# Kernel tuning notes

Hardware: AMD Instinct MI355X
Metric: run time of the kernel (lower is better)

Reference implementation:

```python
import jax, jax.numpy as jnp
import numpy as np

B, S, C, HEADS, EXP = 8, 1024, 256, 8, 4
H = W = 32  # S = H*W
HID = EXP * C
RATES = (1, 6, 12, 18)
EPS = 1e-5


def _conv(x, w, b=None, dilation=1, padding=0):
    out = jax.lax.conv_general_dilated(
        x, w, (1, 1), [(padding, padding), (padding, padding)],
        rhs_dilation=(dilation, dilation),
        dimension_numbers=('NCHW', 'OIHW', 'NCHW'))
    if b is not None:
        out = out + b[None, :, None, None]
    return out


def _bn(x, g, b, m, v):
    # inference-mode BatchNorm2d
    s = (g / jnp.sqrt(v + EPS))[None, :, None, None]
    return (x - m[None, :, None, None]) * s + b[None, :, None, None]


def _ln(x, g, b):
    mu = jnp.mean(x, -1, keepdims=True)
    var = jnp.mean((x - mu) ** 2, -1, keepdims=True)
    return (x - mu) / jnp.sqrt(var + EPS) * g + b


def setup_inputs() -> dict:
    key = jax.random.key(0)
    ks = iter(jax.random.split(key, 64))

    def n(shape, s=0.05):
        return jax.random.normal(next(ks), shape, jnp.float32) * s

    def u(shape):
        return jax.random.uniform(next(ks), shape, jnp.float32, 0.5, 1.5)

    inp = {
        'value': n((B, S, C), 1.0),
        'key': n((B, S, C), 1.0),
        'query': n((B, S, C), 1.0),
        'res': n((B, S, C), 1.0),
        # nn.MultiheadAttention params
        'attn_wi': n((3 * C, C)), 'attn_bi': jnp.zeros((3 * C,)),
        'attn_wo': n((C, C)), 'attn_bo': jnp.zeros((C,)),
        # Modulator params
        'mod_bias': jnp.zeros((1, C, 1, 1)),
        'ca_w1': n((C // 16, C)), 'ca_w2': n((C, C // 16)),
        'pa_w': n((C, C, 1, 1)),
        'pa_bn_g': jnp.ones((C,)), 'pa_bn_b': jnp.zeros((C,)),
        'pa_bn_m': n((C,), 0.1), 'pa_bn_v': u((C,)),
        'sa_w': n((4, C, C, 3, 3)), 'sa_b': jnp.zeros((4, C)),
        'sa_bn_g': jnp.ones((4, C)), 'sa_bn_b': jnp.zeros((4, C)),
        'sa_bn_m': n((4, C), 0.1), 'sa_bn_v': u((4, C)),
        'sa_out_w': n((C, 4 * C, 1, 1)), 'sa_out_b': jnp.zeros((C,)),
        'out_w': n((C, C, 1, 1)), 'out_b': jnp.zeros((C,)),
        'out_bn_g': jnp.ones((C,)), 'out_bn_b': jnp.zeros((C,)),
        'out_bn_m': n((C,), 0.1), 'out_bn_v': u((C,)),
        # LayerNorms
        'ln1_g': jnp.ones((C,)), 'ln1_b': jnp.zeros((C,)),
        'ln2_g': jnp.ones((C,)), 'ln2_b': jnp.zeros((C,)),
        # E_MLP params
        'mlp_w1': n((HID, C)), 'mlp_b1': jnp.zeros((HID,)),
        'dw_w': n((HID, HID, 3, 3), 0.02), 'dw_b': jnp.zeros((HID,)),
        'pw_w': n((HID, HID, 3, 3), 0.02), 'pw_b': jnp.zeros((HID,)),
        'mlp_w2': n((C, HID)), 'mlp_b2': jnp.zeros((C,)),
    }
    return inp


def reference(value, key, query, res,
              attn_wi, attn_bi, attn_wo, attn_bo,
              mod_bias, ca_w1, ca_w2, pa_w,
              pa_bn_g, pa_bn_b, pa_bn_m, pa_bn_v,
              sa_w, sa_b, sa_bn_g, sa_bn_b, sa_bn_m, sa_bn_v,
              sa_out_w, sa_out_b, out_w, out_b,
              out_bn_g, out_bn_b, out_bn_m, out_bn_v,
              ln1_g, ln1_b, ln2_g, ln2_b,
              mlp_w1, mlp_b1, dw_w, dw_b, pw_w, pw_b, mlp_w2, mlp_b2):
    d = C // HEADS
    # SMA arg shuffle: block calls sma(query,key,value) -> SMA(value=query,key=key,query=value)
    # -> nn.MultiheadAttention(query=value_blk, key=key_blk, value=query_blk)
    q = (value @ attn_wi[:C].T + attn_bi[:C]).reshape(B, S, HEADS, d)
    k = (key @ attn_wi[C:2 * C].T + attn_bi[C:2 * C]).reshape(B, S, HEADS, d)
    v = (query @ attn_wi[2 * C:].T + attn_bi[2 * C:]).reshape(B, S, HEADS, d)
    scores = jnp.einsum('bqhd,bkhd->bhqk', q, k) / jnp.sqrt(jnp.float32(d))
    attn = jax.nn.softmax(scores, axis=-1)
    ctx = jnp.einsum('bhqk,bkhd->bqhd', attn, v).reshape(B, S, C)
    msa = ctx @ attn_wo.T + attn_bo                       # [B,S,C]

    x = msa.transpose(0, 2, 1).reshape(B, C, H, W)        # [B,C,H,W]

    # --- Modulator ---
    pa = x * jax.nn.sigmoid(_bn(_conv(x, pa_w), pa_bn_g, pa_bn_b, pa_bn_m, pa_bn_v))
    y = jnp.mean(x, axis=(2, 3))                          # [B,C]
    y = jax.nn.sigmoid(jax.nn.relu(y @ ca_w1.T) @ ca_w2.T)
    ca = x * y[:, :, None, None]
    pa_ca = jax.nn.softmax(pa @ ca, axis=-1)              # [B,C,H,H] (H==W)
    sa_outs = [_bn(jax.nn.relu(_conv(x, sa_w[i], sa_b[i], dilation=r, padding=r)),
                   sa_bn_g[i], sa_bn_b[i], sa_bn_m[i], sa_bn_v[i])
               for i, r in enumerate(RATES)]
    sa = _conv(jnp.concatenate(sa_outs, axis=1), sa_out_w, sa_out_b)
    out = pa_ca @ sa                                      # [B,C,H,W]
    out = _bn(_conv(out, out_w, out_b), out_bn_g, out_bn_b, out_bn_m, out_bn_v)
    syn = out + mod_bias + x                              # residual inside modulator

    attn_seq = syn.reshape(B, C, S).transpose(0, 2, 1)    # [B,S,C]
    q2 = _ln(attn_seq + res, ln1_g, ln1_b)

    # --- E_MLP ---
    h = jax.nn.gelu(q2 @ mlp_w1.T + mlp_b1, approximate=False)  # [B,S,4C]
    hc = h.transpose(0, 2, 1).reshape(B, HID, H, W)
    hc = _conv(hc, dw_w, dw_b, padding=1)
    hc = _conv(hc, pw_w, pw_b, padding=1)
    h2 = hc.reshape(B, HID, S).transpose(0, 2, 1)
    ff = h2 @ mlp_w2.T + mlp_b2
    return _ln(ff + q2, ln2_g, ln2_b)
```

## Files before the change

### kernel.cpp

```cpp
#include <hip/hip_runtime.h>
#include <hip/hip_bf16.h>
#include <math.h>

typedef __attribute__((ext_vector_type(8))) short bf16x8;
typedef __attribute__((ext_vector_type(4))) short bf16x4;
typedef __attribute__((ext_vector_type(4))) float f32x4;

#define MM 8192
#define CC 256

__device__ __forceinline__ short f2bf(float f) {
  unsigned u = __float_as_uint(f);
  u = (u + 0x7FFFu + ((u >> 16) & 1u)) >> 16;
  return (short)u;
}

__device__ __forceinline__ void gload16(const short* g, short* l) {
  __builtin_amdgcn_global_load_lds(
      (const __attribute__((address_space(1))) unsigned int*)(g),
      (__attribute__((address_space(3))) unsigned int*)(l), 16, 0, 0);
}

__global__ __launch_bounds__(256, 2) void convh_k(const short* __restrict__ Ain,
                                                  const short* __restrict__ Wt,
                                                  short* __restrict__ outB,
                                                  const float* __restrict__ bias) {
  extern __shared__ short sm[];
  const int tid = threadIdx.x;
  const int bx = blockIdx.x;
  const int bm = bx >> 3, bn = bx & 7;
  const int l = tid & 63, w = tid >> 6;
  const int wm = w >> 1, wn = w & 1;
  const int lr = l & 15, lg = l >> 4;
  const int lsub = l >> 3;
  const int srcu = (l & 7) ^ lsub;
  const int img = bm >> 3, rbase = (bm & 7) * 4;
  const bf16x8 zv = {0, 0, 0, 0, 0, 0, 0, 0};

  f32x4 acc[4][4];
#pragma unroll
  for (int i = 0; i < 4; ++i)
#pragma unroll
    for (int j = 0; j < 4; ++j) acc[i][j] = (f32x4){0.f, 0.f, 0.f, 0.f};

  const short* wsrc[4];
#pragma unroll
  for (int i = 0; i < 4; ++i) {
    int rowi = (w * 4 + i) * 8 + lsub;
    wsrc[i] = Wt + (size_t)(bn * 128 + rowi) * 1024 + srcu * 8;
  }

  const short* asrc[6]; int apos[6]; bool avalid[6];
#pragma unroll
  for (int i = 0; i < 6; ++i) {
    int ug = tid + i * 256;
    int pos = ug >> 3, u = ug & 7;
    int irow = pos >> 5, px = pos & 31;
    int grow = rbase + irow - 1;
    avalid[i] = ((unsigned)grow < 32u);
    int growc = grow < 0 ? 0 : (grow > 31 ? 31 : grow);
    asrc[i] = Ain + ((size_t)(img * 1024 + growc * 32 + px)) * 1024 + u * 8;
    apos[i] = pos * 64 + ((u ^ (pos & 7)) << 3);
  }

  bf16x8 areg[6];
  auto issueA = [&](int kc) {
#pragma unroll
    for (int i = 0; i < 6; ++i)
      areg[i] = *(const bf16x8*)(asrc[i] + kc * 64);
  };
  auto writeA = [&](int ab) {
    short* abuf = sm + 16384 + ab * 12288;
#pragma unroll
    for (int i = 0; i < 6; ++i)
      *(bf16x8*)(abuf + apos[i]) = avalid[i] ? areg[i] : zv;
  };
  auto issueW = [&](int kc, int tap, int wb) {
    short* base = sm + wb * 8192;
    size_t wo = (size_t)tap * 1048576 + (size_t)kc * 64;
#pragma unroll
    for (int i = 0; i < 4; ++i)
      gload16(wsrc[i] + wo, base + (w * 4 + i) * 512);
  };
  auto compute = [&](int dy, int dx, const short* bA, const short* bB) {
    __builtin_amdgcn_s_setprio(1);
#pragma unroll
    for (int ks = 0; ks < 64; ks += 32) {
      const int u = (ks >> 3) + lg;
      bf16x8 af[4], bfr[4];
#pragma unroll
      for (int mt = 0; mt < 4; ++mt) {
        int px = (mt & 1) * 16 + lr;
        int ipx = px + dx;
        bool okx = ((unsigned)ipx < 32u);
        int pos = (wm * 2 + (mt >> 1) + 1 + dy) * 32 + (ipx & 31);
        bf16x8 v = *(const bf16x8*)&bA[pos * 64 + ((u ^ (pos & 7)) << 3)];
        af[mt] = okx ? v : zv;
      }
#pragma unroll
      for (int nt = 0; nt < 4; ++nt)
        bfr[nt] = *(const bf16x8*)&bB[(wn * 64 + nt * 16 + lr) * 64 + ((u ^ (lr & 7)) << 3)];
#pragma unroll
      for (int mt = 0; mt < 4; ++mt)
#pragma unroll
        for (int nt = 0; nt < 4; ++nt)
          acc[mt][nt] = __builtin_amdgcn_mfma_f32_16x16x32_bf16(af[mt], bfr[nt], acc[mt][nt], 0, 0, 0);
    }
    __builtin_amdgcn_s_setprio(0);
  };

  issueA(0);
  issueW(0, 0, 0);
  issueW(0, 1, 1);
  asm volatile("s_waitcnt vmcnt(4)" ::: "memory");
  writeA(0);
  asm volatile("s_waitcnt lgkmcnt(0)" ::: "memory");

  for (int kc = 0; kc < 16; ++kc) {
    const int ab = kc & 1;
    const short* bA = sm + 16384 + ab * 12288;
#pragma unroll
    for (int tap = 0; tap < 9; ++tap) {
      const int wb = (kc + tap) & 1;
      const short* bB = sm + wb * 8192;
      if (tap == 7) {
        if (kc < 15) asm volatile("s_waitcnt vmcnt(10)" ::: "memory");
        else         asm volatile("s_waitcnt vmcnt(4)" ::: "memory");
      } else if (tap == 8) {
        if (kc < 15) asm volatile("s_waitcnt vmcnt(4)" ::: "memory");
        else         asm volatile("s_waitcnt vmcnt(0)" ::: "memory");
      } else {
        asm volatile("s_waitcnt vmcnt(4)" ::: "memory");
      }
      asm volatile("s_barrier" ::: "memory");
      compute(tap / 3 - 1, tap % 3 - 1, bA, bB);
      asm volatile("s_barrier" ::: "memory");
      if (tap <= 6) {
        if (tap == 6 && kc < 15) issueA(kc + 1);
        issueW(kc, tap + 2, wb);
      } else if (tap == 7) {
        if (kc < 15) issueW(kc + 1, 0, wb);
      } else {
        if (kc < 15) {
          writeA(ab ^ 1);
          asm volatile("s_waitcnt lgkmcnt(0)" ::: "memory");
          issueW(kc + 1, 1, wb);
        }
      }
    }
  }

#pragma unroll
  for (int nt = 0; nt < 4; ++nt) {
    const int col = bn * 128 + wn * 64 + nt * 16 + lr;
    const float bi = bias[col];
#pragma unroll
    for (int mt = 0; mt < 4; ++mt) {
      const int row0 = bm * 128 + wm * 64 + mt * 16 + lg * 4;
#pragma unroll
      for (int j = 0; j < 4; ++j)
        outB[(size_t)(row0 + j) * 1024 + col] = f2bf(acc[mt][nt][j] + bi);
    }
  }
}

struct GP {
  const short* A; const short* W; float* outF; short* outB; float* outT;
  const float* bias; const float* scale; const float* shift; const float* aux;
  const short* zero;
  long aZStride, wZStride, oZStride;
  int N, Kc, ldA, ldOut, outColOff, outZOff;
  int dil0, dil1, dil2, dil3;
  int T, nkcs;
};

template<int TAPS, int EPI, int OUTMODE, int TSTORE, int HALF>
__global__ __launch_bounds__(256, 2) void gemmd_k(GP p) {
  extern __shared__ short sm[];
  constexpr int RG   = HALF ? 2 : 4;
  constexpr int MT   = HALF ? 2 : 4;
  constexpr int NT   = HALF ? 2 : 4;
  constexpr int WTs  = HALF ? 32 : 64;
  constexpr int BMr  = HALF ? 64 : 128;
  constexpr int BNr  = HALF ? 64 : 128;
  constexpr int BSTR = HALF ? 8192 : 16384;
  constexpr int BOFF = HALF ? 4096 : 8192;
  const int tid = threadIdx.x;
  const int bx = blockIdx.x, bz = blockIdx.z;
  const int bm = HALF ? (bx >> 2) : (bx & 63);
  const int bn = HALF ? (bx & 3) : (bx >> 6);
  const int l = tid & 63, w = tid >> 6;
  const int wm = w >> 1, wn = w & 1;
  const int lr = l & 15, lg = l >> 4;
  const int lsub = l >> 3;
  const int srcu = (l & 7) ^ lsub;

  const short* Abase = p.A + (size_t)bz * p.aZStride;
  const short* Wbase = p.W + (size_t)bz * p.wZStride;
  const int dil = (TAPS == 9)
      ? (bz == 0 ? p.dil0 : bz == 1 ? p.dil1 : bz == 2 ? p.dil2 : p.dil3) : 1;

  f32x4 acc[MT][NT];
#pragma unroll
  for (int i = 0; i < MT; ++i)
#pragma unroll
    for (int j = 0; j < NT; ++j) acc[i][j] = (f32x4){0.f, 0.f, 0.f, 0.f};

  int rowi[RG], prow[RG], bimg[RG], py[RG], px[RG];
  const short* wsrc[RG];
#pragma unroll
  for (int i = 0; i < RG; ++i) {
    rowi[i] = (w * RG + i) * 8 + lsub;
    prow[i] = bm * BMr + rowi[i];
    bimg[i] = prow[i] >> 10; py[i] = (prow[i] >> 5) & 31; px[i] = prow[i] & 31;
    wsrc[i] = Wbase + (size_t)(bn * BNr + rowi[i]) * p.Kc + srcu * 8;
  }
  const size_t wTap = (size_t)p.N * p.Kc;
  const int nkcMask = (1 << p.nkcs) - 1;

  auto issue = [&](int t, int buf) {
    const int tap = t >> p.nkcs;
    const int kc = t & nkcMask;
    short* base = sm + buf * BSTR;
    if (TAPS == 1) {
#pragma unroll
      for (int i = 0; i < RG; ++i)
        gload16(Abase + (size_t)prow[i] * p.ldA + kc * 64 + srcu * 8,
                base + (w * RG + i) * 512);
    } else {
      const int dy = (tap / 3 - 1) * dil, dx = (tap % 3 - 1) * dil;
#pragma unroll
      for (int i = 0; i < RG; ++i) {
        int yy = py[i] + dy, xx = px[i] + dx;
        bool ok = ((unsigned)yy < 32u) & ((unsigned)xx < 32u);
        const short* a = ok
            ? Abase + (size_t)((bimg[i] << 10) + (yy << 5) + xx) * p.ldA + kc * 64
            : p.zero;
        gload16(a + srcu * 8, base + (w * RG + i) * 512);
      }
    }
    short* bbase = base + BOFF;
    const size_t wo = (size_t)tap * wTap + kc * 64;
#pragma unroll
    for (int i = 0; i < RG; ++i)
      gload16(wsrc[i] + wo, bbase + (w * RG + i) * 512);
  };

  auto compute = [&](int buf) {
    const short* bA = sm + buf * BSTR;
    const short* bB = bA + BOFF;
    __builtin_amdgcn_s_setprio(1);
#pragma unroll
    for (int ks = 0; ks < 64; ks += 32) {
      const int u = (ks >> 3) + lg;
      bf16x8 af[MT], bfr[NT];
#pragma unroll
      for (int mt = 0; mt < MT; ++mt)
        af[mt] = *(bf16x8*)&bA[(wm * WTs + mt * 16 + lr) * 64 + ((u ^ (lr & 7)) << 3)];
#pragma unroll
      for (int nt = 0; nt < NT; ++nt)
        bfr[nt] = *(bf16x8*)&bB[(wn * WTs + nt * 16 + lr) * 64 + ((u ^ (lr & 7)) << 3)];
#pragma unroll
      for (int mt = 0; mt < MT; ++mt)
#pragma unroll
        for (int nt = 0; nt < NT; ++nt)
          acc[mt][nt] = __builtin_amdgcn_mfma_f32_16x16x32_bf16(af[mt], bfr[nt], acc[mt][nt], 0, 0, 0);
    }
    __builtin_amdgcn_s_setprio(0);
  };

  issue(0, 0);
  if (p.T > 1) issue(1, 1);
  int cur = 0;
  for (int t = 0; t < p.T; ++t) {
    if (t + 1 < p.T) {
      if (HALF) asm volatile("s_waitcnt vmcnt(4)" ::: "memory");
      else      asm volatile("s_waitcnt vmcnt(8)" ::: "memory");
    } else {
      asm volatile("s_waitcnt vmcnt(0)" ::: "memory");
    }
    asm volatile("s_barrier" ::: "memory");
    compute(cur);
    asm volatile("s_barrier" ::: "memory");
    if (t + 2 < p.T) issue(t + 2, cur);
    cur ^= 1;
  }

  float* outF = p.outF + (size_t)bz * p.oZStride;
  short* outB = p.outB + (size_t)bz * p.oZStride;
#pragma unroll
  for (int nt = 0; nt < NT; ++nt) {
    const int col = bn * BNr + wn * WTs + nt * 16 + lr;
    const int gcol = p.outColOff + bz * p.outZOff + col;
    const float bi = (p.bias != nullptr) ? p.bias[bz * p.N + col] : 0.f;
    float scl = 0.f, shf = 0.f;
    if (EPI == 3 || EPI == 4 || EPI == 5) {
      scl = p.scale[bz * p.N + col]; shf = p.shift[bz * p.N + col];
    }
#pragma unroll
    for (int mt = 0; mt < MT; ++mt) {
      const int row0 = bm * BMr + wm * WTs + mt * 16 + lg * 4;
      f32x4 vv;
#pragma unroll
      for (int j = 0; j < 4; ++j) {
        const long row = row0 + j;
        float v = acc[mt][nt][j];
        if (EPI == 1 || EPI == 2 || EPI == 3) v += bi;
        if (EPI == 2) v = 0.5f * v * (1.f + erff(v * 0.70710678118654752f));
        if (EPI == 3) { v = fmaxf(v, 0.f); v = v * scl + shf; }
        if (EPI == 4) {
          float t2 = v * scl + shf;
          float sg = 1.f / (1.f + __expf(-t2));
          v = p.aux[row * 256 + col] * sg;
        }
        if (EPI == 5) v = v * scl + shf + p.aux[row * 256 + col];
        vv[j] = v;
        if (OUTMODE == 0 || OUTMODE == 2) outF[row * (long)p.ldOut + gcol] = v;
        if (OUTMODE == 1 || OUTMODE == 2) outB[row * (long)p.ldOut + gcol] = f2bf(v);
      }
      if (TSTORE) {
        float* t = p.outT + ((size_t)(row0 >> 10) * 256 + gcol) * 1024 + (row0 & 1023);
        *(f32x4*)t = vv;
      }
    }
  }
}

__global__ __launch_bounds__(256) void attn_k(const short* qb, const short* kb,
                                              const short* vb, short* ctx) {
  __shared__ short lK[128 * 40];
  __shared__ short lVt[32 * 136];
  __shared__ short lP[4][16 * 136];
  const int tid = threadIdx.x;
  const int qt = blockIdx.x;
  const int bh = blockIdx.y;
  const int b = bh >> 3, h = bh & 7;
  const int l = tid & 63, wv = tid >> 6;
  const int lr = l & 15, lg = l >> 4;
  const float SC = 0.17677669529663687f;

  const int qrow = qt * 64 + wv * 16 + lr;
  const bf16x8 qf = *(const bf16x8*)(qb + ((size_t)(b * 1024 + qrow)) * 256 + h * 32 + lg * 8);

  f32x4 o0 = {0.f,0.f,0.f,0.f}, o1 = {0.f,0.f,0.f,0.f};
  float m[4] = {-1e30f, -1e30f, -1e30f, -1e30f};
  float lsum[4] = {0.f, 0.f, 0.f, 0.f};

  for (int ch = 0; ch < 8; ++ch) {
    __syncthreads();
    {
      const int keyi = tid >> 1, d0 = (tid & 1) * 16;
      const short* src = kb + ((size_t)(b * 1024 + ch * 128 + keyi)) * 256 + h * 32 + d0;
      short* dst = &lK[keyi * 40 + d0];
      *(bf16x8*)dst = *(const bf16x8*)src;
      *(bf16x8*)(dst + 8) = *(const bf16x8*)(src + 8);
    }
    {
      const int keyi = tid >> 1, d0 = (tid & 1) * 16;
      const short* src = vb + ((size_t)(b * 1024 + ch * 128 + keyi)) * 256 + h * 32 + d0;
      short tmp[16];
      *(bf16x8*)tmp = *(const bf16x8*)src;
      *(bf16x8*)(tmp + 8) = *(const bf16x8*)(src + 8);
#pragma unroll
      for (int j = 0; j < 16; ++j) lVt[(d0 + j) * 136 + keyi] = tmp[j];
    }
    __syncthreads();

    f32x4 sc[8];
#pragma unroll
    for (int jt = 0; jt < 8; ++jt) {
      bf16x8 bfr = *(bf16x8*)&lK[(jt * 16 + lr) * 40 + lg * 8];
      sc[jt] = __builtin_amdgcn_mfma_f32_16x16x32_bf16(qf, bfr, (f32x4){0.f,0.f,0.f,0.f}, 0, 0, 0);
      sc[jt] *= SC;
    }
#pragma unroll
    for (int j = 0; j < 4; ++j) {
      float rm = -1e30f;
#pragma unroll
      for (int jt = 0; jt < 8; ++jt) rm = fmaxf(rm, sc[jt][j]);
      rm = fmaxf(rm, __shfl_xor(rm, 1));
      rm = fmaxf(rm, __shfl_xor(rm, 2));
      rm = fmaxf(rm, __shfl_xor(rm, 4));
      rm = fmaxf(rm, __shfl_xor(rm, 8));
      float mn = fmaxf(m[j], rm);
      float alpha = exp2f((m[j] - mn) * 1.44269504088896f);
      m[j] = mn;
      float rs = 0.f;
#pragma unroll
      for (int jt = 0; jt < 8; ++jt) {
        float pv = exp2f((sc[jt][j] - mn) * 1.44269504088896f);
        sc[jt][j] = pv;
        rs += pv;
      }
      rs += __shfl_xor(rs, 1); rs += __shfl_xor(rs, 2);
      rs += __shfl_xor(rs, 4); rs += __shfl_xor(rs, 8);
      lsum[j] = lsum[j] * alpha + rs;
      o0[j] *= alpha; o1[j] *= alpha;
      const int prw = lg * 4 + j;
#pragma unroll
      for (int jt = 0; jt < 8; ++jt) lP[wv][prw * 136 + jt * 16 + lr] = f2bf(sc[jt][j]);
    }
#pragma unroll
    for (int kc = 0; kc < 4; ++kc) {
      bf16x8 pf = *(bf16x8*)&lP[wv][lr * 136 + kc * 32 + lg * 8];
      bf16x8 v0 = *(bf16x8*)&lVt[lr * 136 + kc * 32 + lg * 8];
      bf16x8 v1 = *(bf16x8*)&lVt[(16 + lr) * 136 + kc * 32 + lg * 8];
      o0 = __builtin_amdgcn_mfma_f32_16x16x32_bf16(pf, v0, o0, 0, 0, 0);
      o1 = __builtin_amdgcn_mfma_f32_16x16x32_bf16(pf, v1, o1, 0, 0, 0);
    }
  }
  const size_t orow = (size_t)(b * 1024 + qt * 64 + wv * 16);
#pragma unroll
  for (int j = 0; j < 4; ++j) {
    float inv = 1.f / lsum[j];
    ctx[(orow + lg * 4 + j) * 256 + h * 32 + lr]      = f2bf(o0[j] * inv);
    ctx[(orow + lg * 4 + j) * 256 + h * 32 + 16 + lr] = f2bf(o1[j] * inv);
  }
}

struct PP {
  const float* value; const float* key; const float* query;
  const float* attn_wi; const float* attn_wo; const float* pa_w;
  const float* sa_out_w; const float* out_w; const float* mlp_w1; const float* mlp_w2;
  const float* sa_w; const float* dw_w; const float* pw_w;
  short* vkq; short* w_awi; short* w_awo; short* w_pa; short* w_saou;
  short* w_out; short* w_mlp1; short* w_mlp2; short* w_sa; short* wdw; short* wpw;
  short* zbuf;
  const float* pg; const float* pb; const float* pm; const float* pv;
  const float* sg; const float* sb; const float* smean; const float* svar;
  const float* og; const float* ob; const float* om; const float* ov;
  const float* conv_ob; const float* mbias; float* bn;
};

__global__ __launch_bounds__(256) void prep_k(PP p) {
  const int b = blockIdx.x, t = threadIdx.x;
  auto cvt = [&](const float* s, short* d, int b0) {
    int i = (b - b0) * 256 + t;
    f32x4 v = ((const f32x4*)s)[i];
    bf16x4 o;
    o[0] = f2bf(v[0]); o[1] = f2bf(v[1]); o[2] = f2bf(v[2]); o[3] = f2bf(v[3]);
    ((bf16x4*)d)[i] = o;
  };
  auto tap = [&](const float* s, short* d, int n, int b0) {
    int i = (b - b0) * 256 + t;
    if (i >= n) return;
    const float* sp = s + (size_t)i * 9;
    float v[9];
#pragma unroll
    for (int k = 0; k < 9; ++k) v[k] = sp[k];
#pragma unroll
    for (int k = 0; k < 9; ++k) d[(size_t)k * n + i] = f2bf(v[k]);
  };
  if (b < 2048)        cvt(p.value, p.vkq, 0);
  else if (b < 4096)   cvt(p.key,   p.vkq + (size_t)MM * 256, 2048);
  else if (b < 6144)   cvt(p.query, p.vkq + (size_t)2 * MM * 256, 4096);
  else if (b < 6336)   cvt(p.attn_wi,  p.w_awi, 6144);
  else if (b < 6400)   cvt(p.attn_wo,  p.w_awo, 6336);
  else if (b < 6464)   cvt(p.pa_w,     p.w_pa, 6400);
  else if (b < 6720)   cvt(p.sa_out_w, p.w_saou, 6464);
  else if (b < 6784)   cvt(p.out_w,    p.w_out, 6720);
  else if (b < 7040)   cvt(p.mlp_w1,   p.w_mlp1, 6784);
  else if (b < 7296)   cvt(p.mlp_w2,   p.w_mlp2, 7040);
  else if (b < 8320) {
    int i4 = (b - 7296) >> 8;
    tap(p.sa_w + (size_t)i4 * 589824, p.w_sa + (size_t)i4 * 589824, 65536,
        7296 + i4 * 256);
  }
  else if (b < 12416)  tap(p.dw_w, p.wdw, 1048576, 8320);
  else if (b < 16512)  tap(p.pw_w, p.wpw, 1048576, 12416);
  else if (b == 16512) {
#pragma unroll
    for (int j = 0; j < 8; ++j) p.zbuf[t * 8 + j] = 0;
  } else {
    int c = t;
    float s = p.pg[c] / sqrtf(p.pv[c] + 1e-5f);
    p.bn[c] = s;
    p.bn[256 + c] = p.pb[c] - p.pm[c] * s;
    for (int i = 0; i < 4; ++i) {
      int idx = i * 256 + c;
      float ss = p.sg[idx] / sqrtf(p.svar[idx] + 1e-5f);
      p.bn[512 + idx] = ss;
      p.bn[1536 + idx] = p.sb[idx] - p.smean[idx] * ss;
    }
    float os = p.og[c] / sqrtf(p.ov[c] + 1e-5f);
    p.bn[2560 + c] = os;
    p.bn[2816 + c] = p.ob[c] - p.om[c] * os + p.conv_ob[c] * os + p.mbias[c];
  }
}

__global__ __launch_bounds__(256) void tposeb_k(const float* src, short* dst) {
  __shared__ float tile[32][33];
  int pc = blockIdx.x, cc = blockIdx.y, b = blockIdx.z;
  int tx = threadIdx.x & 31, ty = threadIdx.x >> 5;
  const float* s = src + ((size_t)b * 256 + cc * 32) * 1024 + pc * 32;
#pragma unroll
  for (int k = 0; k < 4; ++k)
    tile[ty + 8 * k][tx] = s[(ty + 8 * k) * 1024 + tx];
  __syncthreads();
  short* d = dst + ((size_t)b * 1024 + pc * 32) * 256 + cc * 32;
#pragma unroll
  for (int k = 0; k < 4; ++k)
    d[(ty + 8 * k) * 256 + tx] = f2bf(tile[tx][ty + 8 * k]);
}

__global__ __launch_bounds__(256) void camean_k(const float* x, float* partial) {
  int blk = blockIdx.x, c = threadIdx.x;
  const float* px = x + ((size_t)blk * 64) * 256 + c;
  float s = 0.f;
#pragma unroll 4
  for (int r = 0; r < 64; ++r) s += px[(size_t)r * 256];
  partial[blk * 256 + c] = s;
}

__global__ __launch_bounds__(256) void ca2_k(const float* partial, const float* w1,
                                             const float* w2, float* y2) {
  __shared__ float ly[256];
  __shared__ float ly1[16];
  int b = blockIdx.x, c = threadIdx.x;
  float s = 0.f;
#pragma unroll
  for (int j = 0; j < 16; ++j) s += partial[(b * 16 + j) * 256 + c];
  ly[c] = s * (1.f / 1024.f);
  __syncthreads();
  if (c < 16) {
    float a = 0.f;
    const float* wp = w1 + c * 256;
    for (int i = 0; i < 256; ++i) a += ly[i] * wp[i];
    ly1[c] = fmaxf(a, 0.f);
  }
  __syncthreads();
  float a = 0.f;
  const float* wp = w2 + c * 16;
#pragma unroll
  for (int j = 0; j < 16; ++j) a += ly1[j] * wp[j];
  y2[b * 256 + c] = 1.f / (1.f + __expf(-a));
}

__global__ __launch_bounds__(256) void bm1_k(const float* paT, const float* xT,
                                             const float* y2, float* pa_ca) {
  __shared__ float sp[32][33], sx[32][33], so[32][33];
  __shared__ float rinv[32];
  int bc = blockIdx.x, t = threadIdx.x;
  for (int e = t; e < 1024; e += 256) {
    sp[e >> 5][e & 31] = paT[(size_t)bc * 1024 + e];
    sx[e >> 5][e & 31] = xT[(size_t)bc * 1024 + e];
  }
  __syncthreads();
  float yv = y2[bc];
  int i = t >> 3, j0 = (t & 7) * 4;
  float a0 = 0.f, a1 = 0.f, a2 = 0.f, a3 = 0.f;
  for (int k = 0; k < 32; ++k) {
    float pv = sp[i][k];
    a0 += pv * sx[k][j0];     a1 += pv * sx[k][j0 + 1];
    a2 += pv * sx[k][j0 + 2]; a3 += pv * sx[k][j0 + 3];
  }
  so[i][j0] = a0 * yv; so[i][j0 + 1] = a1 * yv;
  so[i][j0 + 2] = a2 * yv; so[i][j0 + 3] = a3 * yv;
  __syncthreads();
  if (t < 32) {
    float mx = -1e30f;
    for (int j = 0; j < 32; ++j) mx = fmaxf(mx, so[t][j]);
    float sum = 0.f;
    for (int j = 0; j < 32; ++j) { float pp = __expf(so[t][j] - mx); so[t][j] = pp; sum += pp; }
    rinv[t] = 1.f / sum;
  }
  __syncthreads();
  for (int e = t; e < 1024; e += 256)
    pa_ca[(size_t)bc * 1024 + e] = so[e >> 5][e & 31] * rinv[e >> 5];
}

__global__ __launch_bounds__(256) void bm2_k(const float* pa_ca, const float* saT, float* moT) {
  __shared__ float sp[32][33], ss[32][33];
  int bc = blockIdx.x, t = threadIdx.x;
  for (int e = t; e < 1024; e += 256) {
    sp[e >> 5][e & 31] = pa_ca[(size_t)bc * 1024 + e];
    ss[e >> 5][e & 31] = saT[(size_t)bc * 1024 + e];
  }
  __syncthreads();
  int i = t >> 3, j0 = (t & 7) * 4;
  float a0 = 0.f, a1 = 0.f, a2 = 0.f, a3 = 0.f;
  for (int k = 0; k < 32; ++k) {
    float pv = sp[i][k];
    a0 += pv * ss[k][j0];     a1 += pv * ss[k][j0 + 1];
    a2 += pv * ss[k][j0 + 2]; a3 += pv * ss[k][j0 + 3];
  }
  size_t base = (size_t)bc * 1024 + i * 32 + j0;
  moT[base] = a0; moT[base + 1] = a1; moT[base + 2] = a2; moT[base + 3] = a3;
}

template<int DUAL>
__global__ __launch_bounds__(256) void ln_k(const float* in, const float* res,
                                            const float* g, const float* bta,
                                            float* out, short* outB) {
  __shared__ float red[8];
  size_t row = blockIdx.x;
  int c = threadIdx.x;
  int wv = c >> 6, lane = c & 63;
  float v = in[row * 256 + c] + res[row * 256 + c];
  float s = v;
  for (int mk = 1; mk < 64; mk <<= 1) s += __shfl_xor(s, mk);
  if (lane == 0) red[wv] = s;
  __syncthreads();
  float mu = (red[0] + red[1] + red[2] + red[3]) * (1.f / 256.f);
  float d = v - mu;
  float q = d * d;
  for (int mk = 1; mk < 64; mk <<= 1) q += __shfl_xor(q, mk);
  if (lane == 0) red[4 + wv] = q;
  __syncthreads();
  float var = (red[4] + red[5] + red[6] + red[7]) * (1.f / 256.f);
  float o = d * rsqrtf(var + 1e-5f) * g[c] + bta[c];
  out[row * 256 + c] = o;
  if (DUAL) outB[row * 256 + c] = f2bf(o);
}

extern "C" void kernel_launch(void* const* d_in, const int* in_sizes, int n_in,
                              void* d_out, int out_size, void* d_ws, size_t ws_size,
                              hipStream_t stream) {
  (void)in_sizes; (void)n_in; (void)out_size; (void)ws_size;
  const float* value    = (const float*)d_in[0];
  const float* key      = (const float*)d_in[1];
  const float* query    = (const float*)d_in[2];
  const float* res      = (const float*)d_in[3];
  const float* attn_wi  = (const float*)d_in[4];
  const float* attn_bi  = (const float*)d_in[5];
  const float* attn_wo  = (const float*)d_in[6];
  const float* attn_bo  = (const float*)d_in[7];
  const float* mod_bias = (const float*)d_in[8];
  const float* ca_w1    = (const float*)d_in[9];
  const float* ca_w2    = (const float*)d_in[10];
  const float* pa_w     = (const float*)d_in[11];
  const float* pa_bn_g  = (const float*)d_in[12];
  const float* pa_bn_b  = (const float*)d_in[13];
  const float* pa_bn_m  = (const float*)d_in[14];
  const float* pa_bn_v  = (const float*)d_in[15];
  const float* sa_w     = (const float*)d_in[16];
  const float* sa_b     = (const float*)d_in[17];
  const float* sa_bn_g  = (const float*)d_in[18];
  const float* sa_bn_b  = (const float*)d_in[19];
  const float* sa_bn_m  = (const float*)d_in[20];
  const float* sa_bn_v  = (const float*)d_in[21];
  const float* sa_out_w = (const float*)d_in[22];
  const float* sa_out_b = (const float*)d_in[23];
  const float* out_w    = (const float*)d_in[24];
  const float* out_b    = (const float*)d_in[25];
  const float* out_bn_g = (const float*)d_in[26];
  const float* out_bn_b = (const float*)d_in[27];
  const float* out_bn_m = (const float*)d_in[28];
  const float* out_bn_v = (const float*)d_in[29];
  const float* ln1_g    = (const float*)d_in[30];
  const float* ln1_b    = (const float*)d_in[31];
  const float* ln2_g    = (const float*)d_in[32];
  const float* ln2_b    = (const float*)d_in[33];
  const float* mlp_w1   = (const float*)d_in[34];
  const float* mlp_b1   = (const float*)d_in[35];
  const float* dw_w     = (const float*)d_in[36];
  const float* dw_b     = (const float*)d_in[37];
  const float* pw_w     = (const float*)d_in[38];
  const float* pw_b     = (const float*)d_in[39];
  const float* mlp_w2   = (const float*)d_in[40];
  const float* mlp_b2   = (const float*)d_in[41];

  char* ws = (char*)d_ws;
  const size_t MB = 1024 * 1024;
  char* A = ws + 0 * MB;
  char* Bx = ws + 16 * MB;
  char* Cx = ws + 32 * MB;
  float* xbuf  = (float*)(ws + 40 * MB);
  short* xbf   = (short*)(ws + 48 * MB);
  char* Fx = ws + 52 * MB;
  float* q2buf = (float*)(ws + 60 * MB);
  short* q2B   = (short*)(ws + 68 * MB);
  short* wdw   = (short*)(ws + 72 * MB);
  short* wpw   = (short*)(ws + 90 * MB);
  size_t o = 108 * MB;
  short* w_awi  = (short*)(ws + o); o += 768 * 256 * 2;
  short* w_awo  = (short*)(ws + o); o += 256 * 256 * 2;
  short* w_pa   = (short*)(ws + o); o += 256 * 256 * 2;
  short* w_sa   = (short*)(ws + o); o += (size_t)4 * 9 * 256 * 256 * 2;
  short* w_saou = (short*)(ws + o); o += 256 * 1024 * 2;
  short* w_out  = (short*)(ws + o); o += 256 * 256 * 2;
  short* w_mlp1 = (short*)(ws + o); o += 1024 * 256 * 2;
  short* w_mlp2 = (short*)(ws + o); o += 256 * 1024 * 2;
  float* bn     = (float*)(ws + o); o += 3072 * 4;
  float* y2buf  = (float*)(ws + o); o += 8 * 256 * 4;
  float* capart = (float*)(ws + o); o += 128 * 256 * 4;
  short* zbuf   = (short*)(ws + o); o += 2048 * 2;

  short* vkq  = (short*)A;
  short* qkv  = (short*)Bx;
  short* ctxB = (short*)Cx;
  float* xT   = (float*)A;
  float* paT  = (float*)(A + 8 * MB);
  float* pa_ca = (float*)Bx;
  short* saCat = (short*)A;
  float* saT  = (float*)Cx;
  float* moT  = (float*)Fx;
  short* modB = (short*)Cx;
  float* synBuf = (float*)Fx;
  short* hB   = (short*)A;
  short* hc1B = (short*)Bx;
  short* h2B  = (short*)A;
  float* ffBuf = (float*)Cx;

  const int LDSB = 2 * 16384 * 2;
  const int LDSH = 2 * 8192 * 2;
  const int LDSC = 40960 * 2;
  hipFuncSetAttribute((const void*)gemmd_k<1, 1, 1, 0, 1>, hipFuncAttributeMaxDynamicSharedMemorySize, LDSH);
  hipFuncSetAttribute((const void*)gemmd_k<1, 1, 2, 1, 1>, hipFuncAttributeMaxDynamicSharedMemorySize, LDSH);
  hipFuncSetAttribute((const void*)gemmd_k<1, 4, 3, 1, 1>, hipFuncAttributeMaxDynamicSharedMemorySize, LDSH);
  hipFuncSetAttribute((const void*)gemmd_k<9, 3, 1, 0, 0>, hipFuncAttributeMaxDynamicSharedMemorySize, LDSB);
  hipFuncSetAttribute((const void*)gemmd_k<1, 1, 3, 1, 1>, hipFuncAttributeMaxDynamicSharedMemorySize, LDSH);
  hipFuncSetAttribute((const void*)gemmd_k<1, 5, 0, 0, 1>, hipFuncAttributeMaxDynamicSharedMemorySize, LDSH);
  hipFuncSetAttribute((const void*)gemmd_k<1, 2, 1, 0, 0>, hipFuncAttributeMaxDynamicSharedMemorySize, LDSB);
  hipFuncSetAttribute((const void*)gemmd_k<1, 1, 0, 0, 1>, hipFuncAttributeMaxDynamicSharedMemorySize, LDSH);
  hipFuncSetAttribute((const void*)convh_k, hipFuncAttributeMaxDynamicSharedMemorySize, LDSC);

  PP pp;
  pp.value = value; pp.key = key; pp.query = query;
  pp.attn_wi = attn_wi; pp.attn_wo = attn_wo; pp.pa_w = pa_w;
  pp.sa_out_w = sa_out_w; pp.out_w = out_w; pp.mlp_w1 = mlp_w1; pp.mlp_w2 = mlp_w2;
  pp.sa_w = sa_w; pp.dw_w = dw_w; pp.pw_w = pw_w;
  pp.vkq = vkq; pp.w_awi = w_awi; pp.w_awo = w_awo; pp.w_pa = w_pa;
  pp.w_saou = w_saou; pp.w_out = w_out; pp.w_mlp1 = w_mlp1; pp.w_mlp2 = w_mlp2;
  pp.w_sa = w_sa; pp.wdw = wdw; pp.wpw = wpw; pp.zbuf = zbuf;
  pp.pg = pa_bn_g; pp.pb = pa_bn_b; pp.pm = pa_bn_m; pp.pv = pa_bn_v;
  pp.sg = sa_bn_g; pp.sb = sa_bn_b; pp.smean = sa_bn_m; pp.svar = sa_bn_v;
  pp.og = out_bn_g; pp.ob = out_bn_b; pp.om = out_bn_m; pp.ov = out_bn_v;
  pp.conv_ob = out_b; pp.mbias = mod_bias; pp.bn = bn;
  prep_k<<<16514, 256, 0, stream>>>(pp);

  GP g;
  g.zero = zbuf; g.scale = nullptr; g.shift = nullptr; g.aux = nullptr;
  g.aZStride = 0; g.wZStride = 0; g.oZStride = 0;
  g.outColOff = 0; g.outZOff = 0;
  g.dil0 = 1; g.dil1 = 1; g.dil2 = 1; g.dil3 = 1;
  g.outF = nullptr; g.outB = nullptr; g.outT = nullptr;

  g.A = vkq; g.W = w_awi; g.outB = qkv; g.bias = attn_bi;
  g.N = 256; g.Kc = 256; g.ldA = 256; g.ldOut = 256; g.T = 4; g.nkcs = 2;
  g.aZStride = (size_t)MM * 256; g.wZStride = 256 * 256; g.oZStride = (size_t)MM * 256;
  gemmd_k<1, 1, 1, 0, 1><<<dim3(512, 1, 3), 256, LDSH, stream>>>(g);
  g.aZStride = 0; g.wZStride = 0; g.oZStride = 0;

  attn_k<<<dim3(16, 64), 256, 0, stream>>>(qkv, qkv + (size_t)MM * 256,
                                           qkv + (size_t)2 * MM * 256, ctxB);

  g.A = ctxB; g.W = w_awo; g.outF = xbuf; g.outB = xbf; g.outT = xT; g.bias = attn_bo;
  gemmd_k<1, 1, 2, 1, 1><<<dim3(512), 256, LDSH, stream>>>(g);

  g.A = xbf; g.W = w_pa; g.outF = nullptr; g.outB = nullptr; g.outT = paT; g.bias = nullptr;
  g.scale = bn; g.shift = bn + 256; g.aux = xbuf;
  gemmd_k<1, 4, 3, 1, 1><<<dim3(512), 256, LDSH, stream>>>(g);
  g.scale = nullptr; g.shift = nullptr; g.aux = nullptr;

  camean_k<<<128, 256, 0, stream>>>(xbuf, capart);
  ca2_k<<<8, 256, 0, stream>>>(capart, ca_w1, ca_w2, y2buf);
  bm1_k<<<2048, 256, 0, stream>>>(paT, xT, y2buf, pa_ca);

  g.A = xbf; g.W = w_sa; g.outB = saCat; g.outF = nullptr; g.outT = nullptr;
  g.bias = sa_b; g.scale = bn + 512; g.shift = bn + 1536;
  g.ldOut = 1024; g.outZOff = 256; g.wZStride = (size_t)9 * 256 * 256;
  g.dil0 = 1; g.dil1 = 6; g.dil2 = 12; g.dil3 = 18;
  g.T = 36; g.nkcs = 2;
  gemmd_k<9, 3, 1, 0, 0><<<dim3(128, 1, 4), 256, LDSB, stream>>>(g);
  g.outZOff = 0; g.wZStride = 0; g.scale = nullptr; g.shift = nullptr;
  g.dil0 = 1; g.dil1 = 1; g.dil2 = 1; g.dil3 = 1;

  g.A = saCat; g.W = w_saou; g.outB = nullptr; g.outT = saT; g.bias = sa_out_b;
  g.N = 256; g.Kc = 1024; g.ldA = 1024; g.ldOut = 256; g.T = 16; g.nkcs = 4;
  gemmd_k<1, 1, 3, 1, 1><<<dim3(512), 256, LDSH, stream>>>(g);

  bm2_k<<<2048, 256, 0, stream>>>(pa_ca, saT, moT);
  tposeb_k<<<dim3(32, 8, 8), 256, 0, stream>>>(moT, modB);

  g.A = modB; g.W = w_out; g.outF = synBuf; g.outT = nullptr; g.bias = nullptr;
  g.scale = bn + 2560; g.shift = bn + 2816; g.aux = xbuf;
  g.N = 256; g.Kc = 256; g.ldA = 256; g.ldOut = 256; g.T = 4; g.nkcs = 2;
  gemmd_k<1, 5, 0, 0, 1><<<dim3(512), 256, LDSH, stream>>>(g);
  g.scale = nullptr; g.shift = nullptr; g.aux = nullptr;

  ln_k<1><<<8192, 256, 0, stream>>>(synBuf, res, ln1_g, ln1_b, q2buf, q2B);

  g.A = q2B; g.W = w_mlp1; g.outB = hB; g.outF = nullptr; g.bias = mlp_b1;
  g.N = 1024; g.Kc = 256; g.ldA = 256; g.ldOut = 1024; g.T = 4; g.nkcs = 2;
  gemmd_k<1, 2, 1, 0, 0><<<dim3(512), 256, LDSB, stream>>>(g);

  convh_k<<<dim3(512), 256, LDSC, stream>>>(hB, wdw, hc1B, dw_b);

  convh_k<<<dim3(512), 256, LDSC, stream>>>(hc1B, wpw, h2B, pw_b);

  g.A = h2B; g.W = w_mlp2; g.outF = ffBuf; g.outB = nullptr; g.bias = mlp_b2;
  g.N = 256; g.Kc = 1024; g.ldA = 1024; g.ldOut = 256; g.T = 16; g.nkcs = 4;
  gemmd_k<1, 1, 0, 0, 1><<<dim3(512), 256, LDSH, stream>>>(g);

  ln_k<0><<<8192, 256, 0, stream>>>(ffBuf, q2buf, ln2_g, ln2_b, (float*)d_out, nullptr);
}
```

Before: 508.2 us.

## Store transposed GEMM outputs as bf16 and prefetch K/V in attention

The transposed outputs (xT, paT, saT) that feed the batched small-matmul kernels are now written and read as bf16 instead of fp32, halving their memory traffic. The attention kernel also loads the next K/V chunk into registers while computing on the current one, then writes it to LDS behind a barrier, so global load latency overlaps with MFMA work. The cost is lower precision on those intermediates and higher register pressure in the attention kernel.

```diff
diff --git a/kernel.cpp b/kernel.cpp
--- a/kernel.cpp
+++ b/kernel.cpp
@@ -13,6 +13,9 @@
   unsigned u = __float_as_uint(f);
   u = (u + 0x7FFFu + ((u >> 16) & 1u)) >> 16;
   return (short)u;
+}
+__device__ __forceinline__ float b2f(short s) {
+  return __uint_as_float(((unsigned)(unsigned short)s) << 16);
 }
 
 __device__ __forceinline__ void gload16(const short* g, short* l) {
@@ -165,7 +168,7 @@
 }
 
 struct GP {
-  const short* A; const short* W; float* outF; short* outB; float* outT;
+  const short* A; const short* W; float* outF; short* outB; short* outTB;
   const float* bias; const float* scale; const float* shift; const float* aux;
   const short* zero;
   long aZStride, wZStride, oZStride;
@@ -319,8 +322,10 @@
         if (OUTMODE == 1 || OUTMODE == 2) outB[row * (long)p.ldOut + gcol] = f2bf(v);
       }
       if (TSTORE) {
-        float* t = p.outT + ((size_t)(row0 >> 10) * 256 + gcol) * 1024 + (row0 & 1023);
-        *(f32x4*)t = vv;
+        short* t = p.outTB + ((size_t)(row0 >> 10) * 256 + gcol) * 1024 + (row0 & 1023);
+        bf16x4 s4;
+        s4[0] = f2bf(vv[0]); s4[1] = f2bf(vv[1]); s4[2] = f2bf(vv[2]); s4[3] = f2bf(vv[3]);
+        *(bf16x4*)t = s4;
       }
     }
   }
@@ -338,6 +343,7 @@
   const int l = tid & 63, wv = tid >> 6;
   const int lr = l & 15, lg = l >> 4;
   const float SC = 0.17677669529663687f;
+  const int keyi = tid >> 1, d0 = (tid & 1) * 16;
 
   const int qrow = qt * 64 + wv * 16 + lr;
   const bf16x8 qf = *(const bf16x8*)(qb + ((size_t)(b * 1024 + qrow)) * 256 + h * 32 + lg * 8);
@@ -345,26 +351,33 @@
   f32x4 o0 = {0.f,0.f,0.f,0.f}, o1 = {0.f,0.f,0.f,0.f};
   float m[4] = {-1e30f, -1e30f, -1e30f, -1e30f};
   float lsum[4] = {0.f, 0.f, 0.f, 0.f};
+  bf16x8 kr0, kr1, vr0, vr1;
+
+  auto issueKV = [&](int ch) {
+    const short* srck = kb + ((size_t)(b * 1024 + ch * 128 + keyi)) * 256 + h * 32 + d0;
+    kr0 = *(const bf16x8*)srck;
+    kr1 = *(const bf16x8*)(srck + 8);
+    const short* srcv = vb + ((size_t)(b * 1024 + ch * 128 + keyi)) * 256 + h * 32 + d0;
+    vr0 = *(const bf16x8*)srcv;
+    vr1 = *(const bf16x8*)(srcv + 8);
+  };
+  auto writeKV = [&]() {
+    short* dst = &lK[keyi * 40 + d0];
+    *(bf16x8*)dst = kr0;
+    *(bf16x8*)(dst + 8) = kr1;
+    short tmp[16];
+    *(bf16x8*)tmp = vr0;
+    *(bf16x8*)(tmp + 8) = vr1;
+#pragma unroll
+    for (int j = 0; j < 16; ++j) lVt[(d0 + j) * 136 + keyi] = tmp[j];
+  };
+
+  issueKV(0);
+  writeKV();
+  __syncthreads();
 
   for (int ch = 0; ch < 8; ++ch) {
-    __syncthreads();
-    {
-      const int keyi = tid >> 1, d0 = (tid & 1) * 16;
-      const short* src = kb + ((size_t)(b * 1024 + ch * 128 + keyi)) * 256 + h * 32 + d0;
-      short* dst = &lK[keyi * 40 + d0];
-      *(bf16x8*)dst = *(const bf16x8*)src;
-      *(bf16x8*)(dst + 8) = *(const bf16x8*)(src + 8);
-    }
-    {
-      const int keyi = tid >> 1, d0 = (tid & 1) * 16;
-      const short* src = vb + ((size_t)(b * 1024 + ch * 128 + keyi)) * 256 + h * 32 + d0;
-      short tmp[16];
-      *(bf16x8*)tmp = *(const bf16x8*)src;
-      *(bf16x8*)(tmp + 8) = *(const bf16x8*)(src + 8);
-#pragma unroll
-      for (int j = 0; j < 16; ++j) lVt[(d0 + j) * 136 + keyi] = tmp[j];
-    }
-    __syncthreads();
+    if (ch < 7) issueKV(ch + 1);
 
     f32x4 sc[8];
 #pragma unroll
@@ -408,6 +421,9 @@
       o0 = __builtin_amdgcn_mfma_f32_16x16x32_bf16(pf, v0, o0, 0, 0, 0);
       o1 = __builtin_amdgcn_mfma_f32_16x16x32_bf16(pf, v1, o1, 0, 0, 0);
     }
+    __syncthreads();
+    if (ch < 7) writeKV();
+    __syncthreads();
   }
   const size_t orow = (size_t)(b * 1024 + qt * 64 + wv * 16);
 #pragma unroll
@@ -536,14 +552,14 @@
   y2[b * 256 + c] = 1.f / (1.f + __expf(-a));
 }
 
-__global__ __launch_bounds__(256) void bm1_k(const float* paT, const float* xT,
+__global__ __launch_bounds__(256) void bm1_k(const short* paT, const short* xT,
                                              const float* y2, float* pa_ca) {
   __shared__ float sp[32][33], sx[32][33], so[32][33];
   __shared__ float rinv[32];
   int bc = blockIdx.x, t = threadIdx.x;
   for (int e = t; e < 1024; e += 256) {
-    sp[e >> 5][e & 31] = paT[(size_t)bc * 1024 + e];
-    sx[e >> 5][e & 31] = xT[(size_t)bc * 1024 + e];
+    sp[e >> 5][e & 31] = b2f(paT[(size_t)bc * 1024 + e]);
+    sx[e >> 5][e & 31] = b2f(xT[(size_t)bc * 1024 + e]);
   }
   __syncthreads();
   float yv = y2[bc];
@@ -569,12 +585,12 @@
     pa_ca[(size_t)bc * 1024 + e] = so[e >> 5][e & 31] * rinv[e >> 5];
 }
 
-__global__ __launch_bounds__(256) void bm2_k(const float* pa_ca, const float* saT, float* moT) {
+__global__ __launch_bounds__(256) void bm2_k(const float* pa_ca, const short* saT, float* moT) {
   __shared__ float sp[32][33], ss[32][33];
   int bc = blockIdx.x, t = threadIdx.x;
   for (int e = t; e < 1024; e += 256) {
     sp[e >> 5][e & 31] = pa_ca[(size_t)bc * 1024 + e];
-    ss[e >> 5][e & 31] = saT[(size_t)bc * 1024 + e];
+    ss[e >> 5][e & 31] = b2f(saT[(size_t)bc * 1024 + e]);
   }
   __syncthreads();
   int i = t >> 3, j0 = (t & 7) * 4;
@@ -689,11 +705,11 @@
   short* vkq  = (short*)A;
   short* qkv  = (short*)Bx;
   short* ctxB = (short*)Cx;
-  float* xT   = (float*)A;
-  float* paT  = (float*)(A + 8 * MB);
+  short* xT   = (short*)A;
+  short* paT  = (short*)(A + 8 * MB);
   float* pa_ca = (float*)Bx;
   short* saCat = (short*)A;
-  float* saT  = (float*)Cx;
+  short* saT  = (short*)Cx;
   float* moT  = (float*)Fx;
   short* modB = (short*)Cx;
   float* synBuf = (float*)Fx;
@@ -734,7 +750,7 @@
   g.aZStride = 0; g.wZStride = 0; g.oZStride = 0;
   g.outColOff = 0; g.outZOff = 0;
   g.dil0 = 1; g.dil1 = 1; g.dil2 = 1; g.dil3 = 1;
-  g.outF = nullptr; g.outB = nullptr; g.outT = nullptr;
+  g.outF = nullptr; g.outB = nullptr; g.outTB = nullptr;
 
   g.A = vkq; g.W = w_awi; g.outB = qkv; g.bias = attn_bi;
   g.N = 256; g.Kc = 256; g.ldA = 256; g.ldOut = 256; g.T = 4; g.nkcs = 2;
@@ -745,10 +761,10 @@
   attn_k<<<dim3(16, 64), 256, 0, stream>>>(qkv, qkv + (size_t)MM * 256,
                                            qkv + (size_t)2 * MM * 256, ctxB);
 
-  g.A = ctxB; g.W = w_awo; g.outF = xbuf; g.outB = xbf; g.outT = xT; g.bias = attn_bo;
+  g.A = ctxB; g.W = w_awo; g.outF = xbuf; g.outB = xbf; g.outTB = xT; g.bias = attn_bo;
   gemmd_k<1, 1, 2, 1, 1><<<dim3(512), 256, LDSH, stream>>>(g);
 
-  g.A = xbf; g.W = w_pa; g.outF = nullptr; g.outB = nullptr; g.outT = paT; g.bias = nullptr;
+  g.A = xbf; g.W = w_pa; g.outF = nullptr; g.outB = nullptr; g.outTB = paT; g.bias = nullptr;
   g.scale = bn; g.shift = bn + 256; g.aux = xbuf;
   gemmd_k<1, 4, 3, 1, 1><<<dim3(512), 256, LDSH, stream>>>(g);
   g.scale = nullptr; g.shift = nullptr; g.aux = nullptr;
@@ -757,7 +773,7 @@
   ca2_k<<<8, 256, 0, stream>>>(capart, ca_w1, ca_w2, y2buf);
   bm1_k<<<2048, 256, 0, stream>>>(paT, xT, y2buf, pa_ca);
 
-  g.A = xbf; g.W = w_sa; g.outB = saCat; g.outF = nullptr; g.outT = nullptr;
+  g.A = xbf; g.W = w_sa; g.outB = saCat; g.outF = nullptr; g.outTB = nullptr;
   g.bias = sa_b; g.scale = bn + 512; g.shift = bn + 1536;
   g.ldOut = 1024; g.outZOff = 256; g.wZStride = (size_t)9 * 256 * 256;
   g.dil0 = 1; g.dil1 = 6; g.dil2 = 12; g.dil3 = 18;
@@ -766,14 +782,14 @@
   g.outZOff = 0; g.wZStride = 0; g.scale = nullptr; g.shift = nullptr;
   g.dil0 = 1; g.dil1 = 1; g.dil2 = 1; g.dil3 = 1;
 
-  g.A = saCat; g.W = w_saou; g.outB = nullptr; g.outT = saT; g.bias = sa_out_b;
+  g.A = saCat; g.W = w_saou; g.outB = nullptr; g.outTB = saT; g.bias = sa_out_b;
   g.N = 256; g.Kc = 1024; g.ldA = 1024; g.ldOut = 256; g.T = 16; g.nkcs = 4;
   gemmd_k<1, 1, 3, 1, 1><<<dim3(512), 256, LDSH, stream>>>(g);
 
   bm2_k<<<2048, 256, 0, stream>>>(pa_ca, saT, moT);
   tposeb_k<<<dim3(32, 8, 8), 256, 0, stream>>>(moT, modB);
 
-  g.A = modB; g.W = w_out; g.outF = synBuf; g.outT = nullptr; g.bias = nullptr;
+  g.A = modB; g.W = w_out; g.outF = synBuf; g.outTB = nullptr; g.bias = nullptr;
   g.scale = bn + 2560; g.shift = bn + 2816; g.aux = xbuf;
   g.N = 256; g.Kc = 256; g.ldA = 256; g.ldOut = 256; g.T = 4; g.nkcs = 2;
   gemmd_k<1, 5, 0, 0, 1><<<dim3(512), 256, LDSH, stream>>>(g);
```

Measured after the change: 508.9 us. No clear change (+0.1%).
